# Kernel tuning notes

Measured on AMD Instinct MI355X. Metric: run time of the kernel, lower is better.

Reference implementation:

```python
import jax, jax.numpy as jnp
import numpy as np

N = 100000
E = 1600000
F = 64
THETA = (0.6, -0.4, 0.3, -0.2, 0.1)  # k = 5 polynomial coefficients


def setup_inputs() -> dict:
    key = jax.random.key(0)
    kx, ke = jax.random.split(key)
    x = jax.random.normal(kx, (N, F), dtype=jnp.float32)
    edge_index = jax.random.randint(ke, (2, E), 0, N, dtype=jnp.int64)
    return {"x": x, "edge_index": edge_index}


def _l_sym_mul(feat, src, dst, deg_inv_sqrt, n):
    # L_sym * feat = feat - D^{-1/2} A D^{-1/2} feat
    src_norm = feat[src] * deg_inv_sqrt[src]            # [E, F] gather + scale
    agg = jax.ops.segment_sum(src_norm, dst, num_segments=n)  # scatter-add to dst
    return feat - deg_inv_sqrt * agg


def reference(x, edge_index):
    src, dst = edge_index[0], edge_index[1]
    n = x.shape[0]
    # in-degree from dst, clamp to >= 1, D^{-1/2} as [N, 1]
    deg = jax.ops.segment_sum(jnp.ones((src.shape[0],), dtype=x.dtype), dst,
                              num_segments=n)
    deg = jnp.maximum(deg, 1.0)[:, None]
    deg_inv_sqrt = deg ** -0.5

    h_acc = THETA[0] * x
    feat = x
    for k in range(1, len(THETA)):
        feat = _l_sym_mul(feat, src, dst, deg_inv_sqrt, n)
        h_acc = h_acc + THETA[k] * feat
    return h_acc
```

## Files before the change

kernel.cpp:

```cpp
#include <hip/hip_runtime.h>


constexpr int kF = 64;
constexpr int BSHIFT = 8;
constexpr int NB = 1 << BSHIFT;
constexpr int TILE = 4096;
constexpr int KMAX = 512;

static __device__ __forceinline__ float bfl(unsigned u) {
    return __uint_as_float(u << 16);
}
static __device__ __forceinline__ float bfh(unsigned u) {
    return __uint_as_float(u & 0xffff0000u);
}
static __device__ __forceinline__ unsigned f2bf(float f) {
    unsigned u = __float_as_uint(f);
    return (u + 0x7fffu + ((u >> 16) & 1u)) >> 16;
}
static __device__ __forceinline__ unsigned pack2(float a, float b) {
    return f2bf(a) | (f2bf(b) << 16);
}

__global__ void k_zero_i(int* __restrict__ p, int n) {
    int i = blockIdx.x * blockDim.x + threadIdx.x;
    if (i < n) p[i] = 0;
}

__global__ void k_binA(const int* __restrict__ src, const int* __restrict__ dst,
                       unsigned* __restrict__ pairs, int* __restrict__ gcursor,
                       const float4* __restrict__ x4, uint4* __restrict__ xb4,
                       int n8, int E, int K, int cap) {
    __shared__ unsigned sorted[TILE];
    __shared__ int hist[KMAX];
    __shared__ int stmp[KMAX];
    __shared__ int loff[KMAX + 1];
    __shared__ int lcur[KMAX];
    __shared__ int gb[KMAX];
    const int tid = threadIdx.x;
    const long long tb = (long long)blockIdx.x * TILE;
    const int tcount = (int)min((long long)TILE, (long long)E - tb);

    {
        int per = (n8 + gridDim.x - 1) / (int)gridDim.x;
        int b0 = blockIdx.x * per;
        int b1 = min(b0 + per, n8);
        for (int i = b0 + tid; i < b1; i += 512) {
            float4 a = x4[2 * i];
            float4 b = x4[2 * i + 1];
            uint4 o;
            o.x = pack2(a.x, a.y);
            o.y = pack2(a.z, a.w);
            o.z = pack2(b.x, b.y);
            o.w = pack2(b.z, b.w);
            xb4[i] = o;
        }
    }

    hist[tid] = 0;
    __syncthreads();
    for (int i = tid; i < tcount; i += 512)
        atomicAdd(&hist[dst[tb + i] >> BSHIFT], 1);
    __syncthreads();
    int v = hist[tid];
    stmp[tid] = v;
    __syncthreads();
    for (int o = 1; o < KMAX; o <<= 1) {
        int t = (tid >= o) ? stmp[tid - o] : 0;
        __syncthreads();
        stmp[tid] += t;
        __syncthreads();
    }
    loff[tid] = stmp[tid] - v;
    lcur[tid] = stmp[tid] - v;
    gb[tid] = (tid < K) ? atomicAdd(&gcursor[tid], v) : 0;
    if (tid == KMAX - 1) loff[KMAX] = stmp[KMAX - 1];
    __syncthreads();
    for (int i = tid; i < tcount; i += 512) {
        int d = dst[tb + i];
        int s = src[tb + i];
        int b = d >> BSHIFT;
        int pos = atomicAdd(&lcur[b], 1);
        sorted[pos] = ((unsigned)(d & (NB - 1)) << 23) | (unsigned)s;
    }
    __syncthreads();
    for (int i = tid; i < tcount; i += 512) {
        int lo = 0, hi = K - 1;
        while (lo < hi) {
            int mid = (lo + hi + 1) >> 1;
            if (loff[mid] <= i) lo = mid; else hi = mid - 1;
        }
        pairs[(size_t)lo * cap + gb[lo] + (i - loff[lo])] = sorted[i];
    }
}

__global__ void k_binB(const unsigned* __restrict__ pairs, const int* __restrict__ gcursor,
                       int* __restrict__ rp, float* __restrict__ dinv,
                       int* __restrict__ csr, int N, int E, int K, int cap) {
    __shared__ int gsc[KMAX];
    __shared__ int cnt[NB];
    __shared__ int stmp[NB];
    __shared__ int excl[NB];
    __shared__ int cur[NB];
    const int b = blockIdx.x;
    const int tid = threadIdx.x;

    int gv = (tid < K) ? gcursor[tid] : 0;
    gsc[tid] = gv;
    __syncthreads();
    for (int o = 1; o < KMAX; o <<= 1) {
        int t = (tid >= o) ? gsc[tid - o] : 0;
        __syncthreads();
        gsc[tid] += t;
        __syncthreads();
    }
    const int ecnt = gcursor[b];
    const int base = gsc[b] - ecnt;
    const unsigned* bp = pairs + (size_t)b * cap;

    if (tid < NB) cnt[tid] = 0;
    __syncthreads();
    for (int i = tid; i < ecnt; i += 512)
        atomicAdd(&cnt[bp[i] >> 23], 1);
    __syncthreads();
    int v = (tid < NB) ? cnt[tid] : 0;
    if (tid < NB) stmp[tid] = v;
    __syncthreads();
    for (int o = 1; o < NB; o <<= 1) {
        int t = (tid >= o && tid < NB) ? stmp[tid - o] : 0;
        __syncthreads();
        if (tid < NB) stmp[tid] += t;
        __syncthreads();
    }
    if (tid < NB) {
        excl[tid] = stmp[tid] - v;
        cur[tid] = stmp[tid] - v;
    }
    __syncthreads();
    for (int i = tid; i < ecnt; i += 512) {
        unsigned p = bp[i];
        int pos = atomicAdd(&cur[p >> 23], 1);
        csr[base + pos] = (int)(p & 0x7FFFFFu);
    }
    int node = (b << BSHIFT) + tid;
    if (tid < NB && node < N) {
        rp[node] = base + excl[tid];
        dinv[node] = rsqrtf(fmaxf((float)v, 1.0f));
    }
    if (b == K - 1 && tid == 0) rp[N] = E;
}

template <bool FIRST, bool LAST>
__global__ void k_gather(const int* __restrict__ rp, const int* __restrict__ csr,
                         const unsigned short* __restrict__ featin,
                         const float* __restrict__ xf,
                         const float* __restrict__ dinv,
                         unsigned short* __restrict__ featout,
                         float* __restrict__ h,
                         int n, float th0, float theta) {
    int wid = (blockIdx.x * blockDim.x + threadIdx.x) >> 6;
    int lane = threadIdx.x & 63;
    int half = lane >> 5;
    int r = (lane >> 3) & 3;
    int c = lane & 7;
    int node = wid * 2 + half;
    if (wid * 2 >= n) return;
    bool valid = node < n;
    int beg = valid ? rp[node] : 0;
    int end = valid ? rp[node + 1] : 0;
    int len = end - beg;
    int olen = __shfl_xor(len, 32, 64);
    int mlen = (len > olen) ? len : olen;

    float acc[8] = {0.f, 0.f, 0.f, 0.f, 0.f, 0.f, 0.f, 0.f};
    for (int i = 0; i < mlen; i += 8) {
        int j1 = beg + i + r;
        int j2 = j1 + 4;
        bool ok1 = j1 < end;
        bool ok2 = j2 < end;
        int s1 = csr[ok1 ? j1 : 0];
        int s2 = csr[ok2 ? j2 : 0];
        float w1 = ok1 ? dinv[s1] : 0.0f;
        float w2 = ok2 ? dinv[s2] : 0.0f;
        uint4 ra = *(const uint4*)(featin + ((size_t)s1 << 6) + (c << 3));
        uint4 rb = *(const uint4*)(featin + ((size_t)s2 << 6) + (c << 3));
        acc[0] += w1 * bfl(ra.x);
        acc[1] += w1 * bfh(ra.x);
        acc[2] += w1 * bfl(ra.y);
        acc[3] += w1 * bfh(ra.y);
        acc[4] += w1 * bfl(ra.z);
        acc[5] += w1 * bfh(ra.z);
        acc[6] += w1 * bfl(ra.w);
        acc[7] += w1 * bfh(ra.w);
        acc[0] += w2 * bfl(rb.x);
        acc[1] += w2 * bfh(rb.x);
        acc[2] += w2 * bfl(rb.y);
        acc[3] += w2 * bfh(rb.y);
        acc[4] += w2 * bfl(rb.z);
        acc[5] += w2 * bfh(rb.z);
        acc[6] += w2 * bfl(rb.w);
        acc[7] += w2 * bfh(rb.w);
    }
    #pragma unroll
    for (int m = 8; m <= 16; m <<= 1) {
        #pragma unroll
        for (int i = 0; i < 8; ++i)
            acc[i] += __shfl_xor(acc[i], m, 64);
    }

    if (r == 0 && valid) {
        size_t off = ((size_t)node << 6) + (c << 3);
        float f[8];
        if (FIRST) {
            float4 a = *(const float4*)(xf + off);
            float4 b = *(const float4*)(xf + off + 4);
            f[0] = a.x; f[1] = a.y; f[2] = a.z; f[3] = a.w;
            f[4] = b.x; f[5] = b.y; f[6] = b.z; f[7] = b.w;
        } else {
            uint4 rr = *(const uint4*)(featin + off);
            f[0] = bfl(rr.x); f[1] = bfh(rr.x);
            f[2] = bfl(rr.y); f[3] = bfh(rr.y);
            f[4] = bfl(rr.z); f[5] = bfh(rr.z);
            f[6] = bfl(rr.w); f[7] = bfh(rr.w);
        }
        float di = dinv[node];
        float v[8];
        #pragma unroll
        for (int i = 0; i < 8; ++i) v[i] = f[i] - di * acc[i];
        float4 h0, h1;
        if (FIRST) {
            h0 = make_float4(th0 * f[0] + theta * v[0], th0 * f[1] + theta * v[1],
                             th0 * f[2] + theta * v[2], th0 * f[3] + theta * v[3]);
            h1 = make_float4(th0 * f[4] + theta * v[4], th0 * f[5] + theta * v[5],
                             th0 * f[6] + theta * v[6], th0 * f[7] + theta * v[7]);
        } else {
            h0 = *(const float4*)(h + off);
            h1 = *(const float4*)(h + off + 4);
            h0.x += theta * v[0]; h0.y += theta * v[1];
            h0.z += theta * v[2]; h0.w += theta * v[3];
            h1.x += theta * v[4]; h1.y += theta * v[5];
            h1.z += theta * v[6]; h1.w += theta * v[7];
        }
        *(float4*)(h + off) = h0;
        *(float4*)(h + off + 4) = h1;
        if (!LAST) {
            uint4 o;
            o.x = pack2(v[0], v[1]);
            o.y = pack2(v[2], v[3]);
            o.z = pack2(v[4], v[5]);
            o.w = pack2(v[6], v[7]);
            *(uint4*)(featout + off) = o;
        }
    }
}

extern "C" void kernel_launch(void* const* d_in, const int* in_sizes, int n_in,
                              void* d_out, int out_size, void* d_ws, size_t ws_size,
                              hipStream_t stream) {
    const float* x  = (const float*)d_in[0];
    const int*   ei = (const int*)d_in[1];
    const int N = in_sizes[0] / kF;
    const int E = in_sizes[1] / 2;
    const int* src = ei;
    const int* dst = ei + E;
    float* h = (float*)d_out;

    const int K = (N + NB - 1) >> BSHIFT;
    const int cap = 2 * ((E + K - 1) / K);

    char* ws = (char*)d_ws;
    size_t off = 0;
    auto carve = [&](size_t bytes) {
        void* p = ws + off;
        off = (off + bytes + 511) & ~(size_t)511;
        return p;
    };
    int*            gcursor = (int*)carve((size_t)K * 4);
    int*            rp      = (int*)carve((size_t)(N + 1) * 4);
    float*          dinv    = (float*)carve((size_t)N * 4);
    int*            csr     = (int*)carve((size_t)E * 4);
    unsigned short* xb      = (unsigned short*)carve((size_t)N * kF * 2);
    unsigned short* featA   = (unsigned short*)carve((size_t)N * kF * 2);
    unsigned short* featB   = (unsigned short*)carve((size_t)N * kF * 2);
    unsigned*       pairs   = (unsigned*)carve((size_t)K * cap * 4);

    const float theta[5] = {0.6f, -0.4f, 0.3f, -0.2f, 0.1f};

    const int n8 = N * kF / 8;
    k_zero_i<<<1, 512, 0, stream>>>(gcursor, K);
    k_binA<<<(E + TILE - 1) / TILE, 512, 0, stream>>>(src, dst, pairs, gcursor,
                                                      (const float4*)x, (uint4*)xb,
                                                      n8, E, K, cap);
    k_binB<<<K, 512, 0, stream>>>(pairs, gcursor, rp, dinv, csr, N, E, K, cap);

    const int nwaves = (N + 1) / 2;
    const int gblocks = (nwaves + 3) / 4;
    k_gather<true, false><<<gblocks, 256, 0, stream>>>(rp, csr, xb, x, dinv, featA, h,
                                                       N, theta[0], theta[1]);
    k_gather<false, false><<<gblocks, 256, 0, stream>>>(rp, csr, featA, nullptr, dinv, featB, h,
                                                        N, 0.f, theta[2]);
    k_gather<false, false><<<gblocks, 256, 0, stream>>>(rp, csr, featB, nullptr, dinv, featA, h,
                                                        N, 0.f, theta[3]);
    k_gather<false, true><<<gblocks, 256, 0, stream>>>(rp, csr, featA, nullptr, dinv, nullptr, h,
                                                       N, 0.f, theta[4]);
}
```

Measured before the change: 273.9 us.

## Pack edge weights into CSR and simplify binning to direct atomic scatter

k_binA drops its local counting sort, scan and binary search. Each edge now claims a slot in its bucket with a shared atomic and writes straight to the global pairs buffer, which removes several barriers and scan passes but makes the writes less coalesced. The CSR becomes int2 (source, dinv[source]), filled by a new k_wtab kernel, so the four gather passes read the weight with the index instead of doing a dependent dinv lookup. This doubles CSR bytes per edge and adds one extra pass over the edges; the zeroing kernel is also replaced with hipMemsetAsync.

```diff
diff --git a/kernel.cpp b/kernel.cpp
--- a/kernel.cpp
+++ b/kernel.cpp
@@ -21,20 +21,11 @@
     return f2bf(a) | (f2bf(b) << 16);
 }
 
-__global__ void k_zero_i(int* __restrict__ p, int n) {
-    int i = blockIdx.x * blockDim.x + threadIdx.x;
-    if (i < n) p[i] = 0;
-}
-
 __global__ void k_binA(const int* __restrict__ src, const int* __restrict__ dst,
                        unsigned* __restrict__ pairs, int* __restrict__ gcursor,
                        const float4* __restrict__ x4, uint4* __restrict__ xb4,
                        int n8, int E, int K, int cap) {
-    __shared__ unsigned sorted[TILE];
     __shared__ int hist[KMAX];
-    __shared__ int stmp[KMAX];
-    __shared__ int loff[KMAX + 1];
-    __shared__ int lcur[KMAX];
     __shared__ int gb[KMAX];
     const int tid = threadIdx.x;
     const long long tb = (long long)blockIdx.x * TILE;
@@ -61,41 +52,23 @@
     for (int i = tid; i < tcount; i += 512)
         atomicAdd(&hist[dst[tb + i] >> BSHIFT], 1);
     __syncthreads();
-    int v = hist[tid];
-    stmp[tid] = v;
-    __syncthreads();
-    for (int o = 1; o < KMAX; o <<= 1) {
-        int t = (tid >= o) ? stmp[tid - o] : 0;
-        __syncthreads();
-        stmp[tid] += t;
-        __syncthreads();
-    }
-    loff[tid] = stmp[tid] - v;
-    lcur[tid] = stmp[tid] - v;
-    gb[tid] = (tid < K) ? atomicAdd(&gcursor[tid], v) : 0;
-    if (tid == KMAX - 1) loff[KMAX] = stmp[KMAX - 1];
+    int hv = hist[tid];
+    gb[tid] = (tid < K && hv > 0) ? atomicAdd(&gcursor[tid], hv) : 0;
+    hist[tid] = 0;
     __syncthreads();
     for (int i = tid; i < tcount; i += 512) {
         int d = dst[tb + i];
         int s = src[tb + i];
         int b = d >> BSHIFT;
-        int pos = atomicAdd(&lcur[b], 1);
-        sorted[pos] = ((unsigned)(d & (NB - 1)) << 23) | (unsigned)s;
-    }
-    __syncthreads();
-    for (int i = tid; i < tcount; i += 512) {
-        int lo = 0, hi = K - 1;
-        while (lo < hi) {
-            int mid = (lo + hi + 1) >> 1;
-            if (loff[mid] <= i) lo = mid; else hi = mid - 1;
-        }
-        pairs[(size_t)lo * cap + gb[lo] + (i - loff[lo])] = sorted[i];
+        int pos = atomicAdd(&hist[b], 1);
+        pairs[(size_t)b * cap + gb[b] + pos] =
+            ((unsigned)(d & (NB - 1)) << 23) | (unsigned)s;
     }
 }
 
 __global__ void k_binB(const unsigned* __restrict__ pairs, const int* __restrict__ gcursor,
                        int* __restrict__ rp, float* __restrict__ dinv,
-                       int* __restrict__ csr, int N, int E, int K, int cap) {
+                       int2* __restrict__ ecsr, int N, int E, int K, int cap) {
     __shared__ int gsc[KMAX];
     __shared__ int cnt[NB];
     __shared__ int stmp[NB];
@@ -139,7 +112,7 @@
     for (int i = tid; i < ecnt; i += 512) {
         unsigned p = bp[i];
         int pos = atomicAdd(&cur[p >> 23], 1);
-        csr[base + pos] = (int)(p & 0x7FFFFFu);
+        ecsr[base + pos].x = (int)(p & 0x7FFFFFu);
     }
     int node = (b << BSHIFT) + tid;
     if (tid < NB && node < N) {
@@ -149,8 +122,17 @@
     if (b == K - 1 && tid == 0) rp[N] = E;
 }
 
+__global__ void k_wtab(int2* __restrict__ ecsr, const float* __restrict__ dinv, int E) {
+    int e = blockIdx.x * blockDim.x + threadIdx.x;
+    if (e < E) {
+        int2 v = ecsr[e];
+        v.y = __float_as_int(dinv[v.x]);
+        ecsr[e] = v;
+    }
+}
+
 template <bool FIRST, bool LAST>
-__global__ void k_gather(const int* __restrict__ rp, const int* __restrict__ csr,
+__global__ void k_gather(const int* __restrict__ rp, const int2* __restrict__ ecsr,
                          const unsigned short* __restrict__ featin,
                          const float* __restrict__ xf,
                          const float* __restrict__ dinv,
@@ -177,10 +159,12 @@
         int j2 = j1 + 4;
         bool ok1 = j1 < end;
         bool ok2 = j2 < end;
-        int s1 = csr[ok1 ? j1 : 0];
-        int s2 = csr[ok2 ? j2 : 0];
-        float w1 = ok1 ? dinv[s1] : 0.0f;
-        float w2 = ok2 ? dinv[s2] : 0.0f;
+        int2 e1 = ecsr[ok1 ? j1 : 0];
+        int2 e2 = ecsr[ok2 ? j2 : 0];
+        int s1 = e1.x;
+        int s2 = e2.x;
+        float w1 = ok1 ? __int_as_float(e1.y) : 0.0f;
+        float w2 = ok2 ? __int_as_float(e2.y) : 0.0f;
         uint4 ra = *(const uint4*)(featin + ((size_t)s1 << 6) + (c << 3));
         uint4 rb = *(const uint4*)(featin + ((size_t)s2 << 6) + (c << 3));
         acc[0] += w1 * bfl(ra.x);
@@ -277,7 +261,7 @@
     int*            gcursor = (int*)carve((size_t)K * 4);
     int*            rp      = (int*)carve((size_t)(N + 1) * 4);
     float*          dinv    = (float*)carve((size_t)N * 4);
-    int*            csr     = (int*)carve((size_t)E * 4);
+    int2*           ecsr    = (int2*)carve((size_t)E * 8);
     unsigned short* xb      = (unsigned short*)carve((size_t)N * kF * 2);
     unsigned short* featA   = (unsigned short*)carve((size_t)N * kF * 2);
     unsigned short* featB   = (unsigned short*)carve((size_t)N * kF * 2);
@@ -286,20 +270,21 @@
     const float theta[5] = {0.6f, -0.4f, 0.3f, -0.2f, 0.1f};
 
     const int n8 = N * kF / 8;
-    k_zero_i<<<1, 512, 0, stream>>>(gcursor, K);
+    hipMemsetAsync(gcursor, 0, (size_t)K * 4, stream);
     k_binA<<<(E + TILE - 1) / TILE, 512, 0, stream>>>(src, dst, pairs, gcursor,
                                                       (const float4*)x, (uint4*)xb,
                                                       n8, E, K, cap);
-    k_binB<<<K, 512, 0, stream>>>(pairs, gcursor, rp, dinv, csr, N, E, K, cap);
+    k_binB<<<K, 512, 0, stream>>>(pairs, gcursor, rp, dinv, ecsr, N, E, K, cap);
+    k_wtab<<<(E + 511) / 512, 512, 0, stream>>>(ecsr, dinv, E);
 
     const int nwaves = (N + 1) / 2;
     const int gblocks = (nwaves + 3) / 4;
-    k_gather<true, false><<<gblocks, 256, 0, stream>>>(rp, csr, xb, x, dinv, featA, h,
+    k_gather<true, false><<<gblocks, 256, 0, stream>>>(rp, ecsr, xb, x, dinv, featA, h,
                                                        N, theta[0], theta[1]);
-    k_gather<false, false><<<gblocks, 256, 0, stream>>>(rp, csr, featA, nullptr, dinv, featB, h,
+    k_gather<false, false><<<gblocks, 256, 0, stream>>>(rp, ecsr, featA, nullptr, dinv, featB, h,
                                                         N, 0.f, theta[2]);
-    k_gather<false, false><<<gblocks, 256, 0, stream>>>(rp, csr, featB, nullptr, dinv, featA, h,
+    k_gather<false, false><<<gblocks, 256, 0, stream>>>(rp, ecsr, featB, nullptr, dinv, featA, h,
                                                         N, 0.f, theta[3]);
-    k_gather<false, true><<<gblocks, 256, 0, stream>>>(rp, csr, featA, nullptr, dinv, nullptr, h,
+    k_gather<false, true><<<gblocks, 256, 0, stream>>>(rp, ecsr, featA, nullptr, dinv, nullptr, h,
                                                        N, 0.f, theta[4]);
 }
```

New measurement: 286.0 us. 4.4% more time.
